# Kernel tuning notes

Hardware: AMD Instinct MI355X
Metric: run time of the kernel (lower is better)

## Reference

```python
import jax, jax.numpy as jnp
import numpy as np

B, T, D_IN, H, N_CLASSES = 32, 64, 10000, 200, 2


def setup_inputs() -> dict:
    key = jax.random.key(0)
    ks = jax.random.split(key, 16)
    s_in = 1.0 / np.sqrt(H)  # torch nn.RNN init scale
    def u(k, shape):
        return jax.random.uniform(k, shape, jnp.float32, -s_in, s_in)
    inp = {"x": jax.random.normal(ks[0], (B, T, D_IN), jnp.float32)}
    dims = [D_IN, H, H]
    for l in range(3):
        inp[f"W_ih{l}"] = u(ks[1 + 4 * l], (H, dims[l]))
        inp[f"W_hh{l}"] = u(ks[2 + 4 * l], (H, H))
        inp[f"b_ih{l}"] = u(ks[3 + 4 * l], (H,))
        inp[f"b_hh{l}"] = u(ks[4 + 4 * l], (H,))
    inp["fc_w"] = u(ks[13], (N_CLASSES, H))
    inp["fc_b"] = u(ks[14], (N_CLASSES,))
    return inp


def _rnn_layer(x_seq, W_ih, W_hh, b_ih, b_hh):
    # x_seq: [B, T, D] -> hidden sequence [B, T, H]
    pre = jnp.einsum('btd,hd->bth', x_seq, W_ih) + b_ih + b_hh  # input proj batched over time
    h0 = jnp.zeros((x_seq.shape[0], W_hh.shape[0]), x_seq.dtype)

    def step(h, p_t):
        h_new = jnp.tanh(p_t + h @ W_hh.T)
        return h_new, h_new

    _, hs = jax.lax.scan(step, h0, jnp.swapaxes(pre, 0, 1))  # [T, B, H]
    return jnp.swapaxes(hs, 0, 1)


def reference(x, W_ih0, W_hh0, b_ih0, b_hh0, W_ih1, W_hh1, b_ih1, b_hh1,
              W_ih2, W_hh2, b_ih2, b_hh2, fc_w, fc_b):
    h = _rnn_layer(x, W_ih0, W_hh0, b_ih0, b_hh0)
    h = _rnn_layer(h, W_ih1, W_hh1, b_ih1, b_hh1)
    h = _rnn_layer(h, W_ih2, W_hh2, b_ih2, b_hh2)
    last = h[:, -1, :]  # [B, H]; dropout is identity at inference
    logits = last @ fc_w.T + fc_b  # [B, n_classes]
    return logits
```

## Files before the change

kernel.cpp:

```cpp
#include <hip/hip_runtime.h>
#include <hip/hip_bf16.h>


typedef __bf16  bf16x8 __attribute__((ext_vector_type(8)));
typedef float   f32x4  __attribute__((ext_vector_type(4)));

#define HDIM 200
#define BM 128
#define CHUNK_B 26624
#define MFMA(a, b, c) __builtin_amdgcn_mfma_f32_16x16x32_bf16(a, b, c, 0, 0, 0)

__device__ __forceinline__ void glds16(const void* g, void* l) {
    __builtin_amdgcn_global_load_lds(
        (const __attribute__((address_space(1))) unsigned int*)g,
        (__attribute__((address_space(3))) unsigned int*)l, 16, 0, 0);
}

__global__ void pack_w(const float* __restrict__ W, int K, int nkc,
                       __bf16* __restrict__ out)
{
    const int total = nkc * 1664;
    for (int g = blockIdx.x * blockDim.x + threadIdx.x; g < total;
         g += gridDim.x * blockDim.x) {
        const int kc = g / 1664;
        const int o  = g - kc * 1664;
        const int isLo = (o >= 832);
        const int o2 = isLo ? o - 832 : o;
        const int r  = o2 >> 2;
        const int k  = kc * 32 + (o2 & 3) * 8;
        bf16x8 v;
        if (r < HDIM && k < K) {
            const float* p = W + (size_t)r * K + k;
            float4 a = *(const float4*)p, b = *(const float4*)(p + 4);
            float f[8] = {a.x, a.y, a.z, a.w, b.x, b.y, b.z, b.w};
#pragma unroll
            for (int i = 0; i < 8; ++i) {
                __bf16 h = (__bf16)f[i];
                v[i] = isLo ? (__bf16)(f[i] - (float)h) : h;
            }
        } else {
#pragma unroll
            for (int i = 0; i < 8; ++i) v[i] = (__bf16)0.f;
        }
        *(bf16x8*)&out[(size_t)g * 8] = v;
    }
}

__global__ __launch_bounds__(512, 1)
void gemm_pipe(const float* __restrict__ A, int lda, int K,
               const __bf16* __restrict__ Bpack,
               float* __restrict__ Cbase, int per_split, int ksteps)
{
    __shared__ alignas(16) __bf16 Ab[2][8192];
    __shared__ alignas(16) __bf16 Bb[2][13312];

    const int tid = threadIdx.x;
    const int kc0 = blockIdx.y * ksteps;
    const int m0  = blockIdx.x * BM;
    float* __restrict__ C = Cbase + (size_t)blockIdx.y * per_split;

    const int wv = tid >> 6, lane = tid & 63;
    const int r16 = lane & 15, kg = lane >> 4;
    const int mg = wv & 3, ng = wv >> 2;
    const int nt0 = ng * 7, ntw = ng ? 6 : 7;

    const int a_row = tid >> 2;
    const int a_q   = tid & 3;
    const float* Arow = A + (size_t)(m0 + a_row) * lda + a_q * 8;

    f32x4 acc[2][7];
#pragma unroll
    for (int mi = 0; mi < 2; ++mi)
#pragma unroll
        for (int j = 0; j < 7; ++j) acc[mi][j] = (f32x4)0.f;

    float av[8];
    auto loadA = [&](int ks) {
        const int kb = (kc0 + ks) * 32;
        if (kb + a_q * 8 < K) {
            const float* p = Arow + kb;
            float4 x0 = *(const float4*)p, x1 = *(const float4*)(p + 4);
            av[0]=x0.x; av[1]=x0.y; av[2]=x0.z; av[3]=x0.w;
            av[4]=x1.x; av[5]=x1.y; av[6]=x1.z; av[7]=x1.w;
        } else {
#pragma unroll
            for (int i = 0; i < 8; ++i) av[i] = 0.f;
        }
    };
    auto issueB = [&](int ks, int buf) {
        const char* src = (const char*)Bpack + (size_t)(kc0 + ks) * CHUNK_B;
        char* dst = (char*)&Bb[buf][0];
#pragma unroll
        for (int r = 0; r < 3; ++r)
            glds16(src + (r * 512 + tid) * 16, dst + (r * 512 + tid) * 16);
        if (tid < 128)
            glds16(src + (1536 + tid) * 16, dst + (1536 + tid) * 16);
    };

    loadA(0);
    issueB(0, 0);

    for (int ks = 0; ks < ksteps; ++ks) {
        const int cur = ks & 1, nxt = cur ^ 1;
        bf16x8 th, tl;
#pragma unroll
        for (int i = 0; i < 8; ++i) {
            __bf16 h = (__bf16)av[i];
            th[i] = h; tl[i] = (__bf16)(av[i] - (float)h);
        }
        *(bf16x8*)&Ab[cur][a_row * 32 + a_q * 8]        = th;
        *(bf16x8*)&Ab[cur][4096 + a_row * 32 + a_q * 8] = tl;
        __syncthreads();
        if (ks + 1 < ksteps) { issueB(ks + 1, nxt); loadA(ks + 1); }

        const int ao0 = (mg * 32 + r16) * 32 + kg * 8;
        const int ao1 = ao0 + 16 * 32;
        bf16x8 ah0 = *(const bf16x8*)&Ab[cur][ao0];
        bf16x8 al0 = *(const bf16x8*)&Ab[cur][4096 + ao0];
        bf16x8 ah1 = *(const bf16x8*)&Ab[cur][ao1];
        bf16x8 al1 = *(const bf16x8*)&Ab[cur][4096 + ao1];
#pragma unroll
        for (int j = 0; j < 7; ++j) {
            if (j < ntw) {
                const int bo = ((nt0 + j) * 16 + r16) * 32 + kg * 8;
                bf16x8 bh = *(const bf16x8*)&Bb[cur][bo];
                bf16x8 bl = *(const bf16x8*)&Bb[cur][6656 + bo];
                acc[0][j] = MFMA(al0, bh, acc[0][j]);
                acc[0][j] = MFMA(ah0, bl, acc[0][j]);
                acc[0][j] = MFMA(ah0, bh, acc[0][j]);
                acc[1][j] = MFMA(al1, bh, acc[1][j]);
                acc[1][j] = MFMA(ah1, bl, acc[1][j]);
                acc[1][j] = MFMA(ah1, bh, acc[1][j]);
            }
        }
    }

#pragma unroll
    for (int mi = 0; mi < 2; ++mi) {
        const int rb = m0 + (mg * 2 + mi) * 16 + kg * 4;
#pragma unroll
        for (int j = 0; j < 7; ++j) {
            if (j < ntw) {
                const int n = (nt0 + j) * 16 + r16;
                if (n < HDIM)
#pragma unroll
                    for (int r = 0; r < 4; ++r)
                        C[(size_t)(rb + r) * HDIM + n] = acc[mi][j][r];
            }
        }
    }
}

__global__ void reduce_parts(const float* __restrict__ Pp, float* __restrict__ P)
{
    const int i = blockIdx.x * blockDim.x + threadIdx.x;
    if (i < 102400) {
        float4 s = ((const float4*)Pp)[i];
#pragma unroll
        for (int r = 1; r < 16; ++r) {
            float4 v = ((const float4*)Pp)[(size_t)r * 102400 + i];
            s.x += v.x; s.y += v.y; s.z += v.z; s.w += v.w;
        }
        ((float4*)P)[i] = s;
    }
}

__device__ __forceinline__ float fast_tanh(float x) {
    float e = __expf(-2.f * fabsf(x));
    float r = (1.f - e) / (1.f + e);
    return copysignf(r, x);
}

__global__ __launch_bounds__(512, 1)
void rnn_rec(const float* __restrict__ pre,
             const float* __restrict__ Whh,
             const float* __restrict__ bih,
             const float* __restrict__ bhh,
             float* __restrict__ Hout)
{
    const int b   = blockIdx.x;
    const int tid = threadIdx.x;

    __shared__ float preS[64 * HDIM];
    __shared__ float h[HDIM];
    __shared__ float bias[HDIM];
    __shared__ float part[10][HDIM];

    {
        const float4* ps = (const float4*)(pre + (size_t)b * 64 * HDIM);
        float4* pd = (float4*)preS;
        for (int i = tid; i < 3200; i += 512) pd[i] = ps[i];
    }

    const bool act = tid < 500;
    const int g  = tid / 10;
    const int s  = tid - g * 10;
    const int n0 = g * 4;
    const int k0 = s * 20;

    float w[80];
    if (act) {
#pragma unroll
        for (int j = 0; j < 4; ++j) {
            const float* wr = Whh + (size_t)(n0 + j) * HDIM + k0;
#pragma unroll
            for (int i = 0; i < 5; ++i) {
                float4 v = *(const float4*)(wr + i * 4);
                w[j * 20 + i * 4 + 0] = v.x; w[j * 20 + i * 4 + 1] = v.y;
                w[j * 20 + i * 4 + 2] = v.z; w[j * 20 + i * 4 + 3] = v.w;
            }
        }
    }
    if (tid < HDIM) { bias[tid] = bih[tid] + bhh[tid]; h[tid] = 0.f; }
    __syncthreads();

    for (int t = 0; t < 64; ++t) {
        if (act) {
            float a0 = 0.f, a1 = 0.f, a2 = 0.f, a3 = 0.f;
#pragma unroll
            for (int i = 0; i < 5; ++i) {
                float4 hv = *(const float4*)&h[k0 + i * 4];
                a0 += w[ 0 + i*4]*hv.x + w[ 1 + i*4]*hv.y + w[ 2 + i*4]*hv.z + w[ 3 + i*4]*hv.w;
                a1 += w[20 + i*4]*hv.x + w[21 + i*4]*hv.y + w[22 + i*4]*hv.z + w[23 + i*4]*hv.w;
                a2 += w[40 + i*4]*hv.x + w[41 + i*4]*hv.y + w[42 + i*4]*hv.z + w[43 + i*4]*hv.w;
                a3 += w[60 + i*4]*hv.x + w[61 + i*4]*hv.y + w[62 + i*4]*hv.z + w[63 + i*4]*hv.w;
            }
            float4 pv = make_float4(a0, a1, a2, a3);
            *(float4*)&part[s][n0] = pv;
        }
        __syncthreads();
        if (tid < HDIM) {
            float sum = part[0][tid];
#pragma unroll
            for (int r = 1; r < 10; ++r) sum += part[r][tid];
            float v = fast_tanh(sum + preS[t * HDIM + tid] + bias[tid]);
            h[tid] = v;
            Hout[((size_t)b * 64 + t) * HDIM + tid] = v;
        }
        __syncthreads();
    }
}


__global__ void fc_head(const float* __restrict__ Hlast_base,
                        const float* __restrict__ fcw,
                        const float* __restrict__ fcb,
                        float* __restrict__ out)
{
    const int i = threadIdx.x;
    if (i >= 64) return;
    const int b = i >> 1, cls = i & 1;
    const float* hp = Hlast_base + ((size_t)b * 64 + 63) * HDIM;
    const float* fw = fcw + cls * HDIM;
    float s = fcb[cls];
    for (int j = 0; j < HDIM; ++j) s += hp[j] * fw[j];
    out[b * 2 + cls] = s;
}

extern "C" void kernel_launch(void* const* d_in, const int* in_sizes, int n_in,
                              void* d_out, int out_size, void* d_ws, size_t ws_size,
                              hipStream_t stream) {
    const float* x     = (const float*)d_in[0];
    const float* W_ih0 = (const float*)d_in[1];
    const float* W_hh0 = (const float*)d_in[2];
    const float* b_ih0 = (const float*)d_in[3];
    const float* b_hh0 = (const float*)d_in[4];
    const float* W_ih1 = (const float*)d_in[5];
    const float* W_hh1 = (const float*)d_in[6];
    const float* b_ih1 = (const float*)d_in[7];
    const float* b_hh1 = (const float*)d_in[8];
    const float* W_ih2 = (const float*)d_in[9];
    const float* W_hh2 = (const float*)d_in[10];
    const float* b_ih2 = (const float*)d_in[11];
    const float* b_hh2 = (const float*)d_in[12];
    const float* fc_w  = (const float*)d_in[13];
    const float* fc_b  = (const float*)d_in[14];
    float* out = (float*)d_out;

    const size_t PE = (size_t)2048 * HDIM;
    float* P     = (float*)d_ws;
    float* Hbuf  = P + PE;
    float* Hbuf2 = Hbuf + PE;
    float* Ppart = Hbuf2 + PE;
    __bf16* W0p  = (__bf16*)(Ppart + 16 * PE);
    __bf16* W1p  = W0p + (size_t)320 * 13312;
    __bf16* W2p  = W1p + (size_t)7 * 13312;

    pack_w<<<1024, 256, 0, stream>>>(W_ih0, 10000, 320, W0p);
    pack_w<<<46, 256, 0, stream>>>(W_ih1, HDIM, 7, W1p);
    pack_w<<<46, 256, 0, stream>>>(W_ih2, HDIM, 7, W2p);

    gemm_pipe<<<dim3(16, 16), 512, 0, stream>>>(x, 10000, 10000, W0p, Ppart, (int)PE, 20);
    reduce_parts<<<400, 256, 0, stream>>>(Ppart, P);
    rnn_rec<<<32, 512, 0, stream>>>(P, W_hh0, b_ih0, b_hh0, Hbuf);

    gemm_pipe<<<dim3(16, 1), 512, 0, stream>>>(Hbuf, HDIM, HDIM, W1p, P, (int)PE, 7);
    rnn_rec<<<32, 512, 0, stream>>>(P, W_hh1, b_ih1, b_hh1, Hbuf2);

    gemm_pipe<<<dim3(16, 1), 512, 0, stream>>>(Hbuf2, HDIM, HDIM, W2p, P, (int)PE, 7);
    rnn_rec<<<32, 512, 0, stream>>>(P, W_hh2, b_ih2, b_hh2, Hbuf);

    fc_head<<<1, 64, 0, stream>>>(Hbuf, fc_w, fc_b, out);
}
```

Measured before the change: 331.8 us.

## Halve GEMM row tile to double blocks; shuffle-reduce RNN step with one barrier

The GEMM row tile drops from 128 to 64, so the grid doubles to 512 blocks for layer 0 and 32 for layers 1-2, and the per-wave N split is rebalanced to 4/3/3/3 tiles with launch bounds raised to 4 blocks per CU. The recurrent kernel now splits K across 8 lanes and reduces partial dot products with wave shuffles instead of a shared partial array. It double-buffers the hidden state, which removes one of the two barriers per timestep. This cuts LDS traffic and synchronisation on the serial critical path, at the cost of more wasted zero-padded K work (224 vs 200) and lower MFMA reuse per block in the GEMM.

```diff
diff --git a/kernel.cpp b/kernel.cpp
--- a/kernel.cpp
+++ b/kernel.cpp
@@ -3,10 +3,11 @@
 
 
 typedef __bf16  bf16x8 __attribute__((ext_vector_type(8)));
+typedef __bf16  bf16x4 __attribute__((ext_vector_type(4)));
 typedef float   f32x4  __attribute__((ext_vector_type(4)));
 
 #define HDIM 200
-#define BM 128
+#define BM 64
 #define CHUNK_B 26624
 #define MFMA(a, b, c) __builtin_amdgcn_mfma_f32_16x16x32_bf16(a, b, c, 0, 0, 0)
 
@@ -46,12 +47,12 @@
     }
 }
 
-__global__ __launch_bounds__(512, 1)
+__global__ __launch_bounds__(512, 4)
 void gemm_pipe(const float* __restrict__ A, int lda, int K,
                const __bf16* __restrict__ Bpack,
                float* __restrict__ Cbase, int per_split, int ksteps)
 {
-    __shared__ alignas(16) __bf16 Ab[2][8192];
+    __shared__ alignas(16) __bf16 Ab[2][4096];
     __shared__ alignas(16) __bf16 Bb[2][13312];
 
     const int tid = threadIdx.x;
@@ -61,30 +62,29 @@
 
     const int wv = tid >> 6, lane = tid & 63;
     const int r16 = lane & 15, kg = lane >> 4;
-    const int mg = wv & 3, ng = wv >> 2;
-    const int nt0 = ng * 7, ntw = ng ? 6 : 7;
-
-    const int a_row = tid >> 2;
-    const int a_q   = tid & 3;
-    const float* Arow = A + (size_t)(m0 + a_row) * lda + a_q * 8;
-
-    f32x4 acc[2][7];
+    const int mg = wv & 1, ng = wv >> 1;
+    const int nt0 = ng ? 1 + ng * 3 : 0;
+    const int ntw = ng ? 3 : 4;
+
+    const int a_row = tid >> 3;
+    const int a_q   = tid & 7;
+    const float* Arow = A + (size_t)(m0 + a_row) * lda + a_q * 4;
+
+    f32x4 acc[2][4];
 #pragma unroll
     for (int mi = 0; mi < 2; ++mi)
 #pragma unroll
-        for (int j = 0; j < 7; ++j) acc[mi][j] = (f32x4)0.f;
-
-    float av[8];
+        for (int j = 0; j < 4; ++j) acc[mi][j] = (f32x4)0.f;
+
+    float av[4];
     auto loadA = [&](int ks) {
         const int kb = (kc0 + ks) * 32;
-        if (kb + a_q * 8 < K) {
-            const float* p = Arow + kb;
-            float4 x0 = *(const float4*)p, x1 = *(const float4*)(p + 4);
-            av[0]=x0.x; av[1]=x0.y; av[2]=x0.z; av[3]=x0.w;
-            av[4]=x1.x; av[5]=x1.y; av[6]=x1.z; av[7]=x1.w;
+        if (kb + a_q * 4 < K) {
+            float4 x0 = *(const float4*)(Arow + kb);
+            av[0] = x0.x; av[1] = x0.y; av[2] = x0.z; av[3] = x0.w;
         } else {
 #pragma unroll
-            for (int i = 0; i < 8; ++i) av[i] = 0.f;
+            for (int i = 0; i < 4; ++i) av[i] = 0.f;
         }
     };
     auto issueB = [&](int ks, int buf) {
@@ -102,25 +102,25 @@
 
     for (int ks = 0; ks < ksteps; ++ks) {
         const int cur = ks & 1, nxt = cur ^ 1;
-        bf16x8 th, tl;
-#pragma unroll
-        for (int i = 0; i < 8; ++i) {
+        bf16x4 th, tl;
+#pragma unroll
+        for (int i = 0; i < 4; ++i) {
             __bf16 h = (__bf16)av[i];
             th[i] = h; tl[i] = (__bf16)(av[i] - (float)h);
         }
-        *(bf16x8*)&Ab[cur][a_row * 32 + a_q * 8]        = th;
-        *(bf16x8*)&Ab[cur][4096 + a_row * 32 + a_q * 8] = tl;
+        *(bf16x4*)&Ab[cur][a_row * 32 + a_q * 4]        = th;
+        *(bf16x4*)&Ab[cur][2048 + a_row * 32 + a_q * 4] = tl;
         __syncthreads();
         if (ks + 1 < ksteps) { issueB(ks + 1, nxt); loadA(ks + 1); }
 
         const int ao0 = (mg * 32 + r16) * 32 + kg * 8;
         const int ao1 = ao0 + 16 * 32;
         bf16x8 ah0 = *(const bf16x8*)&Ab[cur][ao0];
-        bf16x8 al0 = *(const bf16x8*)&Ab[cur][4096 + ao0];
+        bf16x8 al0 = *(const bf16x8*)&Ab[cur][2048 + ao0];
         bf16x8 ah1 = *(const bf16x8*)&Ab[cur][ao1];
-        bf16x8 al1 = *(const bf16x8*)&Ab[cur][4096 + ao1];
-#pragma unroll
-        for (int j = 0; j < 7; ++j) {
+        bf16x8 al1 = *(const bf16x8*)&Ab[cur][2048 + ao1];
+#pragma unroll
+        for (int j = 0; j < 4; ++j) {
             if (j < ntw) {
                 const int bo = ((nt0 + j) * 16 + r16) * 32 + kg * 8;
                 bf16x8 bh = *(const bf16x8*)&Bb[cur][bo];
@@ -137,9 +137,9 @@
 
 #pragma unroll
     for (int mi = 0; mi < 2; ++mi) {
-        const int rb = m0 + (mg * 2 + mi) * 16 + kg * 4;
-#pragma unroll
-        for (int j = 0; j < 7; ++j) {
+        const int rb = m0 + mg * 32 + mi * 16 + kg * 4;
+#pragma unroll
+        for (int j = 0; j < 4; ++j) {
             if (j < ntw) {
                 const int n = (nt0 + j) * 16 + r16;
                 if (n < HDIM)
@@ -182,9 +182,8 @@
     const int tid = threadIdx.x;
 
     __shared__ float preS[64 * HDIM];
-    __shared__ float h[HDIM];
+    __shared__ alignas(16) float h[2][224];
     __shared__ float bias[HDIM];
-    __shared__ float part[10][HDIM];
 
     {
         const float4* ps = (const float4*)(pre + (size_t)b * 64 * HDIM);
@@ -192,55 +191,57 @@
         for (int i = tid; i < 3200; i += 512) pd[i] = ps[i];
     }
 
-    const bool act = tid < 500;
-    const int g  = tid / 10;
-    const int s  = tid - g * 10;
+    const bool act = tid < 400;
+    const int g  = tid >> 3;
+    const int s  = tid & 7;
     const int n0 = g * 4;
-    const int k0 = s * 20;
-
-    float w[80];
+    const int k0 = s * 28;
+
+    float w[4][28];
     if (act) {
 #pragma unroll
         for (int j = 0; j < 4; ++j) {
-            const float* wr = Whh + (size_t)(n0 + j) * HDIM + k0;
-#pragma unroll
-            for (int i = 0; i < 5; ++i) {
-                float4 v = *(const float4*)(wr + i * 4);
-                w[j * 20 + i * 4 + 0] = v.x; w[j * 20 + i * 4 + 1] = v.y;
-                w[j * 20 + i * 4 + 2] = v.z; w[j * 20 + i * 4 + 3] = v.w;
-            }
-        }
-    }
-    if (tid < HDIM) { bias[tid] = bih[tid] + bhh[tid]; h[tid] = 0.f; }
+            const float* wr = Whh + (size_t)(n0 + j) * HDIM;
+#pragma unroll
+            for (int i = 0; i < 28; ++i) {
+                const int k = k0 + i;
+                w[j][i] = (k < HDIM) ? wr[k] : 0.f;
+            }
+        }
+    }
+    if (tid < HDIM) bias[tid] = bih[tid] + bhh[tid];
+    if (tid < 224) { h[0][tid] = 0.f; h[1][tid] = 0.f; }
     __syncthreads();
 
     for (int t = 0; t < 64; ++t) {
+        const int p = t & 1;
         if (act) {
             float a0 = 0.f, a1 = 0.f, a2 = 0.f, a3 = 0.f;
 #pragma unroll
-            for (int i = 0; i < 5; ++i) {
-                float4 hv = *(const float4*)&h[k0 + i * 4];
-                a0 += w[ 0 + i*4]*hv.x + w[ 1 + i*4]*hv.y + w[ 2 + i*4]*hv.z + w[ 3 + i*4]*hv.w;
-                a1 += w[20 + i*4]*hv.x + w[21 + i*4]*hv.y + w[22 + i*4]*hv.z + w[23 + i*4]*hv.w;
-                a2 += w[40 + i*4]*hv.x + w[41 + i*4]*hv.y + w[42 + i*4]*hv.z + w[43 + i*4]*hv.w;
-                a3 += w[60 + i*4]*hv.x + w[61 + i*4]*hv.y + w[62 + i*4]*hv.z + w[63 + i*4]*hv.w;
-            }
-            float4 pv = make_float4(a0, a1, a2, a3);
-            *(float4*)&part[s][n0] = pv;
+            for (int i = 0; i < 7; ++i) {
+                float4 hv = *(const float4*)&h[p][k0 + i * 4];
+                a0 += w[0][i*4+0]*hv.x + w[0][i*4+1]*hv.y + w[0][i*4+2]*hv.z + w[0][i*4+3]*hv.w;
+                a1 += w[1][i*4+0]*hv.x + w[1][i*4+1]*hv.y + w[1][i*4+2]*hv.z + w[1][i*4+3]*hv.w;
+                a2 += w[2][i*4+0]*hv.x + w[2][i*4+1]*hv.y + w[2][i*4+2]*hv.z + w[2][i*4+3]*hv.w;
+                a3 += w[3][i*4+0]*hv.x + w[3][i*4+1]*hv.y + w[3][i*4+2]*hv.z + w[3][i*4+3]*hv.w;
+            }
+            a0 += __shfl_xor(a0, 1); a1 += __shfl_xor(a1, 1);
+            a2 += __shfl_xor(a2, 1); a3 += __shfl_xor(a3, 1);
+            a0 += __shfl_xor(a0, 2); a1 += __shfl_xor(a1, 2);
+            a2 += __shfl_xor(a2, 2); a3 += __shfl_xor(a3, 2);
+            a0 += __shfl_xor(a0, 4); a1 += __shfl_xor(a1, 4);
+            a2 += __shfl_xor(a2, 4); a3 += __shfl_xor(a3, 4);
+            if (s < 4) {
+                const int n = n0 + s;
+                const float sum = (s == 0) ? a0 : (s == 1) ? a1 : (s == 2) ? a2 : a3;
+                const float v = fast_tanh(sum + preS[t * HDIM + n] + bias[n]);
+                h[p ^ 1][n] = v;
+                Hout[((size_t)b * 64 + t) * HDIM + n] = v;
+            }
         }
         __syncthreads();
-        if (tid < HDIM) {
-            float sum = part[0][tid];
-#pragma unroll
-            for (int r = 1; r < 10; ++r) sum += part[r][tid];
-            float v = fast_tanh(sum + preS[t * HDIM + tid] + bias[tid]);
-            h[tid] = v;
-            Hout[((size_t)b * 64 + t) * HDIM + tid] = v;
-        }
-        __syncthreads();
-    }
-}
-
+    }
+}
 
 __global__ void fc_head(const float* __restrict__ Hlast_base,
                         const float* __restrict__ fcw,
@@ -290,14 +291,14 @@
     pack_w<<<46, 256, 0, stream>>>(W_ih1, HDIM, 7, W1p);
     pack_w<<<46, 256, 0, stream>>>(W_ih2, HDIM, 7, W2p);
 
-    gemm_pipe<<<dim3(16, 16), 512, 0, stream>>>(x, 10000, 10000, W0p, Ppart, (int)PE, 20);
+    gemm_pipe<<<dim3(32, 16), 512, 0, stream>>>(x, 10000, 10000, W0p, Ppart, (int)PE, 20);
     reduce_parts<<<400, 256, 0, stream>>>(Ppart, P);
     rnn_rec<<<32, 512, 0, stream>>>(P, W_hh0, b_ih0, b_hh0, Hbuf);
 
-    gemm_pipe<<<dim3(16, 1), 512, 0, stream>>>(Hbuf, HDIM, HDIM, W1p, P, (int)PE, 7);
+    gemm_pipe<<<dim3(32, 1), 512, 0, stream>>>(Hbuf, HDIM, HDIM, W1p, P, (int)PE, 7);
     rnn_rec<<<32, 512, 0, stream>>>(P, W_hh1, b_ih1, b_hh1, Hbuf2);
 
-    gemm_pipe<<<dim3(16, 1), 512, 0, stream>>>(Hbuf2, HDIM, HDIM, W2p, P, (int)PE, 7);
+    gemm_pipe<<<dim3(32, 1), 512, 0, stream>>>(Hbuf2, HDIM, HDIM, W2p, P, (int)PE, 7);
     rnn_rec<<<32, 512, 0, stream>>>(P, W_hh2, b_ih2, b_hh2, Hbuf);
 
     fc_head<<<1, 64, 0, stream>>>(Hbuf, fc_w, fc_b, out);
```

Result: slower. 394.1 us (+18.8%).
